# Performance work log

Measured on AMD Instinct MI355X. Metric: run time of the kernel, lower is better.

The kernel has to match this reference:

```python
import jax, jax.numpy as jnp
import numpy as np

B, S, E, H = 2, 2048, 1024, 16
DK = E // H


def setup_inputs() -> dict:
    key = jax.random.key(0)
    ks = jax.random.split(key, 10)
    x = jax.random.normal(ks[0], (B, S, E), dtype=jnp.float32)
    mask = jax.random.randint(ks[1], (B, S, S), 0, 2).astype(bool)
    scale = 1.0 / np.sqrt(E)
    def lin(k):
        kw, kb = jax.random.split(k)
        W = jax.random.uniform(kw, (E, E), minval=-scale, maxval=scale, dtype=jnp.float32)
        b = jax.random.uniform(kb, (E,), minval=-scale, maxval=scale, dtype=jnp.float32)
        return W, b
    Wq, bq = lin(ks[2])
    Wk, bk = lin(ks[3])
    Wv, bv = lin(ks[4])
    Wo, bo = lin(ks[5])
    return {"x": x, "mask": mask, "Wq": Wq, "bq": bq, "Wk": Wk, "bk": bk,
            "Wv": Wv, "bv": bv, "Wo": Wo, "bo": bo}


def reference(x, mask, Wq, bq, Wk, bk, Wv, bv, Wo, bo):
    # projections (torch Linear: y = x @ W.T + b)
    q = x @ Wq.T + bq
    k = x @ Wk.T + bk
    v = x @ Wv.T + bv
    # separate heads: [B,S,E] -> [B,H,S,DK]
    def split(t):
        return t.reshape(B, S, H, DK).transpose(0, 2, 1, 3)
    q, k, v = split(q), split(k), split(v)
    scores = jnp.einsum("bhqd,bhkd->bhqk", q, k) / jnp.sqrt(jnp.float32(DK))
    # masked_fill: positions where mask is True get -1e9 (mask broadcast over heads)
    scores = jnp.where(mask[:, None, :, :], jnp.float32(-1e9), scores)
    attn = jax.nn.softmax(scores, axis=-1)  # dropout is identity in eval
    out = jnp.einsum("bhqk,bhkd->bhqd", attn, v)
    out = out.transpose(0, 2, 1, 3).reshape(B, S, E)  # combine heads
    return out @ Wo.T + bo
```

## Files before the change

kernel.cpp:

```cpp
#include <hip/hip_runtime.h>
#include <hip/hip_bf16.h>


typedef __attribute__((ext_vector_type(8))) short short8;
typedef __attribute__((ext_vector_type(4))) float f32x4;

#define MFMA16(a, b, c) __builtin_amdgcn_mfma_f32_16x16x32_bf16(a, b, c, 0, 0, 0)

#define BATCH 2
#define SEQ   2048
#define EMB   1024
#define HEADS 16
#define DKK   64
#define MROWS (BATCH * SEQ)

typedef __hip_bfloat16 bf16;
typedef unsigned long long u64;

static __device__ __forceinline__ short bf16b(float f) {
    union { bf16 h; short s; } u;
    u.h = __float2bfloat16(f);
    return u.s;
}
static __device__ __forceinline__ short8 ld8k(const bf16* p) {
    return *(const short8*)p;
}
static __device__ __forceinline__ short8 ld8kf(const float* p) {
    const f32x4 a = *(const f32x4*)p;
    const f32x4 b = *(const f32x4*)(p + 4);
    short8 r;
    r[0] = bf16b(a[0]); r[1] = bf16b(a[1]); r[2] = bf16b(a[2]); r[3] = bf16b(a[3]);
    r[4] = bf16b(b[0]); r[5] = bf16b(b[1]); r[6] = bf16b(b[2]); r[7] = bf16b(b[3]);
    return r;
}

static __device__ __forceinline__ void glds16(const bf16* g, bf16* l) {
    __builtin_amdgcn_global_load_lds(
        (const __attribute__((address_space(1))) void*)g,
        (__attribute__((address_space(3))) void*)l, 16, 0, 0);
}

__global__ void detect_kernel(const unsigned int* __restrict__ mw,
                              int* __restrict__ flags) {
    __shared__ int mbyte;
    if (threadIdx.x == 0) mbyte = 0;
    __syncthreads();
    int mb = 0;
    for (int i = threadIdx.x; i < 4096; i += 256)
        if (mw[i] > 1u) mb = 1;
    if (mb) atomicOr(&mbyte, 1);
    __syncthreads();
    if (threadIdx.x == 0) { flags[0] = 1; flags[1] = mbyte; }
}

__global__ __launch_bounds__(256) void pack_mask(
        const void* __restrict__ mp, u64* __restrict__ bm,
        const int* __restrict__ flags) {
    const bool m8 = flags[1] != 0;
    const unsigned char* p8 = (const unsigned char*)mp;
    const int* p32 = (const int*)mp;
    const int lane = threadIdx.x & 63;
    const int w = (blockIdx.x * 256 + threadIdx.x) >> 6;
#pragma unroll 4
    for (int i = 0; i < 32; ++i) {
        const int L = i * 4096 + w;
        const size_t e = (size_t)L * 64 + lane;
        const bool v = m8 ? (p8[e] != 0) : (p32[e] != 0);
        const u64 bal = __ballot(v);
        if (lane == 0) {
            const int qg = L >> 5, it = L & 31;
            bm[((qg >> 11) * 32 + it) * 2048 + (qg & 2047)] = bal;
        }
    }
}

__global__ __launch_bounds__(256) void cvt_all(
        const float* __restrict__ x,  const float* __restrict__ wq,
        const float* __restrict__ wk, const float* __restrict__ wv,
        const float* __restrict__ wo,
        bf16* __restrict__ xb,  bf16* __restrict__ wqb,
        bf16* __restrict__ wkb, bf16* __restrict__ wvb,
        bf16* __restrict__ wob) {
    const int bid = blockIdx.x;
    const float* s; bf16* d; int base;
    if (bid < 2048)      { s = x;  d = xb;  base = bid; }
    else if (bid < 2560) { s = wq; d = wqb; base = bid - 2048; }
    else if (bid < 3072) { s = wk; d = wkb; base = bid - 2560; }
    else if (bid < 3584) { s = wv; d = wvb; base = bid - 3072; }
    else                 { s = wo; d = wob; base = bid - 3584; }
    const int i = (base * 256 + threadIdx.x) * 8;
    *(short8*)(d + i) = ld8kf(s + i);
}

__global__ __launch_bounds__(256) void gemm_qkv_staged(
        const bf16* __restrict__ X,
        const bf16* __restrict__ Wq, const bf16* __restrict__ Wk,
        const bf16* __restrict__ Wv,
        const float* __restrict__ bq, const float* __restrict__ bk,
        const float* __restrict__ bv,
        bf16* __restrict__ qo, bf16* __restrict__ ko, bf16* __restrict__ vo) {
    __shared__ bf16 As[128 * 64];
    __shared__ bf16 Bs[128 * 64];

    const int t = threadIdx.x, lane = t & 63;
    const int wv = t >> 6;
    const int mb = blockIdx.x / 24, nb = blockIdx.x % 24;
    const int m0 = mb * 128;
    const int n0g = nb * 128;
    const int sel = n0g >> 10;
    const int n0 = n0g & 1023;
    const bf16* W     = sel == 0 ? Wq : (sel == 1 ? Wk : Wv);
    const float* bias = sel == 0 ? bq : (sel == 1 ? bk : bv);
    bf16* out         = sel == 0 ? qo : (sel == 1 ? ko : vo);

    const int wr = wv >> 1, wc = wv & 1;
    const int m_off = wr * 64, n_off = wc * 64;
    const int l16 = lane & 15, quad = lane >> 4;

    int srow[4], sg[4];
#pragma unroll
    for (int i = 0; i < 4; ++i) {
        const int c = i * 256 + t;
        srow[i] = c >> 3;
        sg[i]   = (c & 7) ^ (srow[i] & 7);
    }

    f32x4 acc[4][4];
#pragma unroll
    for (int i = 0; i < 4; ++i)
#pragma unroll
        for (int j = 0; j < 4; ++j)
            acc[i][j] = (f32x4){0.f, 0.f, 0.f, 0.f};

    for (int kt = 0; kt < 1024; kt += 64) {
#pragma unroll
        for (int i = 0; i < 4; ++i)
            glds16(X + (m0 + srow[i]) * 1024 + kt + sg[i] * 8, As + (i * 256 + t) * 8);
#pragma unroll
        for (int i = 0; i < 4; ++i)
            glds16(W + (n0 + srow[i]) * 1024 + kt + sg[i] * 8, Bs + (i * 256 + t) * 8);
        __syncthreads();
#pragma unroll
        for (int step = 0; step < 2; ++step) {
            short8 af[4], bfr[4];
#pragma unroll
            for (int ii = 0; ii < 4; ++ii) {
                const int row = m_off + ii * 16 + l16;
                const int slot = (step * 4 + quad) ^ (row & 7);
                af[ii] = *(const short8*)(As + row * 64 + slot * 8);
            }
#pragma unroll
            for (int jj = 0; jj < 4; ++jj) {
                const int row = n_off + jj * 16 + l16;
                const int slot = (step * 4 + quad) ^ (row & 7);
                bfr[jj] = *(const short8*)(Bs + row * 64 + slot * 8);
            }
#pragma unroll
            for (int ii = 0; ii < 4; ++ii)
#pragma unroll
                for (int jj = 0; jj < 4; ++jj)
                    acc[ii][jj] = MFMA16(af[ii], bfr[jj], acc[ii][jj]);
        }
        __syncthreads();
    }

#pragma unroll
    for (int j = 0; j < 4; ++j) {
        const int nl = n0 + n_off + j * 16 + l16;
        const float bj = bias[nl];
        const int h = nl >> 6, d = nl & 63;
#pragma unroll
        for (int i = 0; i < 4; ++i) {
#pragma unroll
            for (int r = 0; r < 4; ++r) {
                const int m = m0 + m_off + i * 16 + quad * 4 + r;
                const float v = acc[i][j][r] + bj;
                const int bb = m >> 11, ss = m & 2047;
                const int idx = (sel == 2)
                    ? ((bb * HEADS + h) * DKK + d) * SEQ + ss
                    : ((bb * HEADS + h) * SEQ + ss) * DKK + d;
                out[idx] = __float2bfloat16(v);
            }
        }
    }
}

__global__ __launch_bounds__(256) void gemm_out_staged(
        const bf16* __restrict__ X,
        const bf16* __restrict__ W, const float* __restrict__ bias,
        float* __restrict__ out) {
    __shared__ bf16 As[128 * 64];
    __shared__ bf16 Bs[64 * 64];

    const int t = threadIdx.x, lane = t & 63;
    const int wv = t >> 6;
    const int mb = blockIdx.x >> 4, nb = blockIdx.x & 15;
    const int m0 = mb * 128, n0 = nb * 64;
    const int wr = wv >> 1, wc = wv & 1;
    const int m_off = wr * 64, n_off = wc * 32;
    const int l16 = lane & 15, quad = lane >> 4;

    int srow[4], sg[4];
#pragma unroll
    for (int i = 0; i < 4; ++i) {
        const int c = i * 256 + t;
        srow[i] = c >> 3;
        sg[i]   = (c & 7) ^ (srow[i] & 7);
    }

    f32x4 acc[4][2];
#pragma unroll
    for (int i = 0; i < 4; ++i)
#pragma unroll
        for (int j = 0; j < 2; ++j)
            acc[i][j] = (f32x4){0.f, 0.f, 0.f, 0.f};

    for (int kt = 0; kt < 1024; kt += 64) {
#pragma unroll
        for (int i = 0; i < 4; ++i)
            glds16(X + (m0 + srow[i]) * 1024 + kt + sg[i] * 8, As + (i * 256 + t) * 8);
#pragma unroll
        for (int i = 0; i < 2; ++i)
            glds16(W + (n0 + srow[i]) * 1024 + kt + sg[i] * 8, Bs + (i * 256 + t) * 8);
        __syncthreads();
#pragma unroll
        for (int step = 0; step < 2; ++step) {
            short8 af[4], bfr[2];
#pragma unroll
            for (int ii = 0; ii < 4; ++ii) {
                const int row = m_off + ii * 16 + l16;
                const int slot = (step * 4 + quad) ^ (row & 7);
                af[ii] = *(const short8*)(As + row * 64 + slot * 8);
            }
#pragma unroll
            for (int jj = 0; jj < 2; ++jj) {
                const int row = n_off + jj * 16 + l16;
                const int slot = (step * 4 + quad) ^ (row & 7);
                bfr[jj] = *(const short8*)(Bs + row * 64 + slot * 8);
            }
#pragma unroll
            for (int ii = 0; ii < 4; ++ii)
#pragma unroll
                for (int jj = 0; jj < 2; ++jj)
                    acc[ii][jj] = MFMA16(af[ii], bfr[jj], acc[ii][jj]);
        }
        __syncthreads();
    }

#pragma unroll
    for (int j = 0; j < 2; ++j) {
        const int n = n0 + n_off + j * 16 + l16;
        const float bj = bias[n];
#pragma unroll
        for (int i = 0; i < 4; ++i) {
#pragma unroll
            for (int r = 0; r < 4; ++r) {
                const int m = m0 + m_off + i * 16 + quad * 4 + r;
                out[m * 1024 + n] = acc[i][j][r] + bj;
            }
        }
    }
}

__global__ __launch_bounds__(256, 3) void attn_kernel(
        const bf16* __restrict__ Qw,
        const bf16* __restrict__ Kw,
        const bf16* __restrict__ Vw,
        const u64* __restrict__ bmT,
        bf16* __restrict__ attn_out) {
    const int t = threadIdx.x;
    const int lane = t & 63;
    const int wv   = t >> 6;
    const int l16 = lane & 15, quad = lane >> 4;
    const int h = blockIdx.y, b = blockIdx.z;
    const int bh = b * HEADS + h;
    const int qb = blockIdx.x * 64 + wv * 16;

    const bf16* Q  = Qw + bh * SEQ * DKK;
    const bf16* Kp = Kw + bh * SEQ * DKK;
    const bf16* Vt = Vw + bh * DKK * SEQ;

    __shared__ bf16 Ks[2][4096];
    __shared__ bf16 Vs[2][4096];
    __shared__ bf16 lds_p[4][16][72];

    short8 qf[2];
    qf[0] = ld8k(Q + (qb + l16) * DKK + quad * 8);
    qf[1] = ld8k(Q + (qb + l16) * DKK + 32 + quad * 8);

    f32x4 o[4];
#pragma unroll
    for (int jd = 0; jd < 4; ++jd) o[jd] = (f32x4){0.f, 0.f, 0.f, 0.f};
    float lsum[4] = {0.f, 0.f, 0.f, 0.f};

    int srow[2], sg[2];
#pragma unroll
    for (int i = 0; i < 2; ++i) {
        const int c = i * 256 + t;
        srow[i] = c >> 3;
        sg[i]   = (c & 7) ^ (srow[i] & 7);
    }

#pragma unroll
    for (int i = 0; i < 2; ++i)
        glds16(Kp + srow[i] * DKK + sg[i] * 8, &Ks[0][(i * 256 + t) * 8]);
#pragma unroll
    for (int i = 0; i < 2; ++i)
        glds16(Vt + srow[i] * SEQ + sg[i] * 8, &Vs[0][(i * 256 + t) * 8]);

    const int qrow = qb + quad * 4;
    u64 mc[4];
#pragma unroll
    for (int r = 0; r < 4; ++r)
        mc[r] = bmT[(size_t)(b * 32) * 2048 + qrow + r];

    const float SC = 0.18033688011f;

    for (int it = 0; it < SEQ / 64; ++it) {
        __syncthreads();
        const int nb_ = (it + 1) & 1;
        u64 mn[4];
        if (it < SEQ / 64 - 1) {
            const int ktn = (it + 1) * 64;
#pragma unroll
            for (int i = 0; i < 2; ++i)
                glds16(Kp + (ktn + srow[i]) * DKK + sg[i] * 8, &Ks[nb_][(i * 256 + t) * 8]);
#pragma unroll
            for (int i = 0; i < 2; ++i)
                glds16(Vt + srow[i] * SEQ + ktn + sg[i] * 8, &Vs[nb_][(i * 256 + t) * 8]);
#pragma unroll
            for (int r = 0; r < 4; ++r)
                mn[r] = bmT[(size_t)(b * 32 + it + 1) * 2048 + qrow + r];
        }

        const bf16* Kb = Ks[it & 1];
        const bf16* Vb = Vs[it & 1];

        f32x4 s[4];
#pragma unroll
        for (int j = 0; j < 4; ++j) s[j] = (f32x4){0.f, 0.f, 0.f, 0.f};
#pragma unroll
        for (int t2 = 0; t2 < 2; ++t2)
#pragma unroll
            for (int j = 0; j < 4; ++j) {
                const int row = j * 16 + l16;
                const int slot = (t2 * 4 + quad) ^ (row & 7);
                const short8 kf = *(const short8*)(Kb + row * 64 + slot * 8);
                s[j] = MFMA16(qf[t2], kf, s[j]);
            }

#pragma unroll
        for (int r = 0; r < 4; ++r) {
            const unsigned wlo = ~(unsigned)mc[r];
            const unsigned whi = ~(unsigned)(mc[r] >> 32);
#pragma unroll
            for (int j = 0; j < 4; ++j) {
                const unsigned word = (j < 2) ? wlo : whi;
                const float bitf = (float)((word >> ((j & 1) * 16 + l16)) & 1u);
                const float p = __builtin_exp2f(s[j][r] * SC) * bitf;
                lsum[r] += p;
                lds_p[wv][quad * 4 + r][j * 16 + l16] = __float2bfloat16(p);
            }
        }

#pragma unroll
        for (int t2 = 0; t2 < 2; ++t2) {
            const short8 pf = *(const short8*)(&lds_p[wv][l16][t2 * 32 + quad * 8]);
#pragma unroll
            for (int jd = 0; jd < 4; ++jd) {
                const int row = jd * 16 + l16;
                const int slot = (t2 * 4 + quad) ^ (row & 7);
                const short8 vf = *(const short8*)(Vb + row * 64 + slot * 8);
                o[jd] = MFMA16(pf, vf, o[jd]);
            }
        }
        if (it < SEQ / 64 - 1) {
#pragma unroll
            for (int r = 0; r < 4; ++r) mc[r] = mn[r];
        }
    }

#pragma unroll
    for (int r = 0; r < 4; ++r) {
        float l = lsum[r];
#pragma unroll
        for (int off = 8; off >= 1; off >>= 1)
            l += __shfl_xor(l, off, 16);
        const float inv = 1.0f / l;
        const int q = qb + quad * 4 + r;
#pragma unroll
        for (int jd = 0; jd < 4; ++jd)
            attn_out[(b * SEQ + q) * EMB + h * DKK + jd * 16 + l16] =
                __float2bfloat16(o[jd][r] * inv);
    }
}

extern "C" void kernel_launch(void* const* d_in, const int* in_sizes, int n_in,
                              void* d_out, int out_size, void* d_ws, size_t ws_size,
                              hipStream_t stream) {
    char* ws = (char*)d_ws;
    const size_t MB = 1024 * 1024;
    int*  flags = (int*)ws;
    u64*  bm    = (u64*)(ws + 256);
    bf16* xb    = (bf16*)(ws + 256 + MB);
    bf16* wqb   = (bf16*)(ws + 256 + 9 * MB);
    bf16* wkb   = (bf16*)(ws + 256 + 11 * MB);
    bf16* wvb   = (bf16*)(ws + 256 + 13 * MB);
    bf16* wob   = (bf16*)(ws + 256 + 15 * MB);
    bf16* k_ws  = (bf16*)(ws + 256 + 17 * MB);
    bf16* attn_ws = xb;

    bf16* q_ws = (bf16*)d_out;
    bf16* v_ws = (bf16*)d_out + 4194304;

    detect_kernel<<<1, 256, 0, stream>>>((const unsigned int*)d_in[1], flags);
    pack_mask<<<1024, 256, 0, stream>>>(d_in[1], bm, flags);

    cvt_all<<<4096, 256, 0, stream>>>(
        (const float*)d_in[0], (const float*)d_in[2], (const float*)d_in[4],
        (const float*)d_in[6], (const float*)d_in[8],
        xb, wqb, wkb, wvb, wob);

    gemm_qkv_staged<<<768, 256, 0, stream>>>(
        xb, wqb, wkb, wvb,
        (const float*)d_in[3], (const float*)d_in[5], (const float*)d_in[7],
        q_ws, k_ws, v_ws);

    attn_kernel<<<dim3(SEQ / 64, HEADS, BATCH), 256, 0, stream>>>(
        q_ws, k_ws, v_ws, bm, attn_ws);

    gemm_out_staged<<<512, 256, 0, stream>>>(
        attn_ws, wob, (const float*)d_in[9], (float*)d_out);
}
```

Measured before the change: 300.7 us.

## Double-buffer GEMM K tiles and process two query tiles per attention wave

Both projection GEMMs switch from single-buffered 64-wide K tiles with two barriers per step to double-buffered 32-wide K tiles, so the next tile's global-to-LDS load is issued before the MFMAs on the current one. The attention kernel now gives each wave 32 query rows instead of 16, which halves the grid and reuses each K/V fragment loaded from LDS for two query tiles. The goal is to hide load latency and cut LDS traffic per MFMA, at the cost of more registers, a lower occupancy hint and fewer attention blocks in flight.

```diff
diff --git a/kernel.cpp b/kernel.cpp
--- a/kernel.cpp
+++ b/kernel.cpp
@@ -99,8 +99,8 @@
         const float* __restrict__ bq, const float* __restrict__ bk,
         const float* __restrict__ bv,
         bf16* __restrict__ qo, bf16* __restrict__ ko, bf16* __restrict__ vo) {
-    __shared__ bf16 As[128 * 64];
-    __shared__ bf16 Bs[128 * 64];
+    __shared__ bf16 As[2][128 * 32];
+    __shared__ bf16 Bs[2][128 * 32];
 
     const int t = threadIdx.x, lane = t & 63;
     const int wv = t >> 6;
@@ -117,12 +117,12 @@
     const int m_off = wr * 64, n_off = wc * 64;
     const int l16 = lane & 15, quad = lane >> 4;
 
-    int srow[4], sg[4];
-#pragma unroll
-    for (int i = 0; i < 4; ++i) {
+    int srow[2], sg[2];
+#pragma unroll
+    for (int i = 0; i < 2; ++i) {
         const int c = i * 256 + t;
-        srow[i] = c >> 3;
-        sg[i]   = (c & 7) ^ (srow[i] & 7);
+        srow[i] = c >> 2;
+        sg[i]   = (c & 3) ^ (srow[i] & 3);
     }
 
     f32x4 acc[4][4];
@@ -132,36 +132,45 @@
         for (int j = 0; j < 4; ++j)
             acc[i][j] = (f32x4){0.f, 0.f, 0.f, 0.f};
 
-    for (int kt = 0; kt < 1024; kt += 64) {
-#pragma unroll
-        for (int i = 0; i < 4; ++i)
-            glds16(X + (m0 + srow[i]) * 1024 + kt + sg[i] * 8, As + (i * 256 + t) * 8);
-#pragma unroll
-        for (int i = 0; i < 4; ++i)
-            glds16(W + (n0 + srow[i]) * 1024 + kt + sg[i] * 8, Bs + (i * 256 + t) * 8);
+#pragma unroll
+    for (int i = 0; i < 2; ++i) {
+        glds16(X + (m0 + srow[i]) * 1024 + sg[i] * 8, &As[0][(i * 256 + t) * 8]);
+        glds16(W + (n0 + srow[i]) * 1024 + sg[i] * 8, &Bs[0][(i * 256 + t) * 8]);
+    }
+
+    for (int it = 0; it < 32; ++it) {
         __syncthreads();
-#pragma unroll
-        for (int step = 0; step < 2; ++step) {
-            short8 af[4], bfr[4];
-#pragma unroll
-            for (int ii = 0; ii < 4; ++ii) {
-                const int row = m_off + ii * 16 + l16;
-                const int slot = (step * 4 + quad) ^ (row & 7);
-                af[ii] = *(const short8*)(As + row * 64 + slot * 8);
-            }
-#pragma unroll
-            for (int jj = 0; jj < 4; ++jj) {
-                const int row = n_off + jj * 16 + l16;
-                const int slot = (step * 4 + quad) ^ (row & 7);
-                bfr[jj] = *(const short8*)(Bs + row * 64 + slot * 8);
-            }
-#pragma unroll
-            for (int ii = 0; ii < 4; ++ii)
-#pragma unroll
-                for (int jj = 0; jj < 4; ++jj)
-                    acc[ii][jj] = MFMA16(af[ii], bfr[jj], acc[ii][jj]);
-        }
-        __syncthreads();
+        if (it < 31) {
+            const int ktn = (it + 1) * 32;
+            const int nb_ = (it + 1) & 1;
+#pragma unroll
+            for (int i = 0; i < 2; ++i) {
+                glds16(X + (m0 + srow[i]) * 1024 + ktn + sg[i] * 8,
+                       &As[nb_][(i * 256 + t) * 8]);
+                glds16(W + (n0 + srow[i]) * 1024 + ktn + sg[i] * 8,
+                       &Bs[nb_][(i * 256 + t) * 8]);
+            }
+        }
+        const bf16* Ab = As[it & 1];
+        const bf16* Bb = Bs[it & 1];
+        short8 af[4], bfr[4];
+#pragma unroll
+        for (int ii = 0; ii < 4; ++ii) {
+            const int row = m_off + ii * 16 + l16;
+            const int slot = quad ^ (row & 3);
+            af[ii] = *(const short8*)(Ab + row * 32 + slot * 8);
+        }
+#pragma unroll
+        for (int jj = 0; jj < 4; ++jj) {
+            const int row = n_off + jj * 16 + l16;
+            const int slot = quad ^ (row & 3);
+            bfr[jj] = *(const short8*)(Bb + row * 32 + slot * 8);
+        }
+#pragma unroll
+        for (int ii = 0; ii < 4; ++ii)
+#pragma unroll
+            for (int jj = 0; jj < 4; ++jj)
+                acc[ii][jj] = MFMA16(af[ii], bfr[jj], acc[ii][jj]);
     }
 
 #pragma unroll
@@ -189,8 +198,8 @@
         const bf16* __restrict__ X,
         const bf16* __restrict__ W, const float* __restrict__ bias,
         float* __restrict__ out) {
-    __shared__ bf16 As[128 * 64];
-    __shared__ bf16 Bs[64 * 64];
+    __shared__ bf16 As[2][128 * 32];
+    __shared__ bf16 Bs[2][64 * 32];
 
     const int t = threadIdx.x, lane = t & 63;
     const int wv = t >> 6;
@@ -200,13 +209,15 @@
     const int m_off = wr * 64, n_off = wc * 32;
     const int l16 = lane & 15, quad = lane >> 4;
 
-    int srow[4], sg[4];
-#pragma unroll
-    for (int i = 0; i < 4; ++i) {
+    int srow[2], sg[2];
+#pragma unroll
+    for (int i = 0; i < 2; ++i) {
         const int c = i * 256 + t;
-        srow[i] = c >> 3;
-        sg[i]   = (c & 7) ^ (srow[i] & 7);
-    }
+        srow[i] = c >> 2;
+        sg[i]   = (c & 3) ^ (srow[i] & 3);
+    }
+    const int brow = t >> 2;
+    const int bslot = (t & 3) ^ (brow & 3);
 
     f32x4 acc[4][2];
 #pragma unroll
@@ -215,36 +226,42 @@
         for (int j = 0; j < 2; ++j)
             acc[i][j] = (f32x4){0.f, 0.f, 0.f, 0.f};
 
-    for (int kt = 0; kt < 1024; kt += 64) {
-#pragma unroll
-        for (int i = 0; i < 4; ++i)
-            glds16(X + (m0 + srow[i]) * 1024 + kt + sg[i] * 8, As + (i * 256 + t) * 8);
-#pragma unroll
-        for (int i = 0; i < 2; ++i)
-            glds16(W + (n0 + srow[i]) * 1024 + kt + sg[i] * 8, Bs + (i * 256 + t) * 8);
+#pragma unroll
+    for (int i = 0; i < 2; ++i)
+        glds16(X + (m0 + srow[i]) * 1024 + sg[i] * 8, &As[0][(i * 256 + t) * 8]);
+    glds16(W + (n0 + brow) * 1024 + bslot * 8, &Bs[0][t * 8]);
+
+    for (int it = 0; it < 32; ++it) {
         __syncthreads();
-#pragma unroll
-        for (int step = 0; step < 2; ++step) {
-            short8 af[4], bfr[2];
-#pragma unroll
-            for (int ii = 0; ii < 4; ++ii) {
-                const int row = m_off + ii * 16 + l16;
-                const int slot = (step * 4 + quad) ^ (row & 7);
-                af[ii] = *(const short8*)(As + row * 64 + slot * 8);
-            }
-#pragma unroll
-            for (int jj = 0; jj < 2; ++jj) {
-                const int row = n_off + jj * 16 + l16;
-                const int slot = (step * 4 + quad) ^ (row & 7);
-                bfr[jj] = *(const short8*)(Bs + row * 64 + slot * 8);
-            }
-#pragma unroll
-            for (int ii = 0; ii < 4; ++ii)
-#pragma unroll
-                for (int jj = 0; jj < 2; ++jj)
-                    acc[ii][jj] = MFMA16(af[ii], bfr[jj], acc[ii][jj]);
-        }
-        __syncthreads();
+        if (it < 31) {
+            const int ktn = (it + 1) * 32;
+            const int nb_ = (it + 1) & 1;
+#pragma unroll
+            for (int i = 0; i < 2; ++i)
+                glds16(X + (m0 + srow[i]) * 1024 + ktn + sg[i] * 8,
+                       &As[nb_][(i * 256 + t) * 8]);
+            glds16(W + (n0 + brow) * 1024 + ktn + bslot * 8, &Bs[nb_][t * 8]);
+        }
+        const bf16* Ab = As[it & 1];
+        const bf16* Bb = Bs[it & 1];
+        short8 af[4], bfr[2];
+#pragma unroll
+        for (int ii = 0; ii < 4; ++ii) {
+            const int row = m_off + ii * 16 + l16;
+            const int slot = quad ^ (row & 3);
+            af[ii] = *(const short8*)(Ab + row * 32 + slot * 8);
+        }
+#pragma unroll
+        for (int jj = 0; jj < 2; ++jj) {
+            const int row = n_off + jj * 16 + l16;
+            const int slot = quad ^ (row & 3);
+            bfr[jj] = *(const short8*)(Bb + row * 32 + slot * 8);
+        }
+#pragma unroll
+        for (int ii = 0; ii < 4; ++ii)
+#pragma unroll
+            for (int jj = 0; jj < 2; ++jj)
+                acc[ii][jj] = MFMA16(af[ii], bfr[jj], acc[ii][jj]);
     }
 
 #pragma unroll
@@ -262,7 +279,7 @@
     }
 }
 
-__global__ __launch_bounds__(256, 3) void attn_kernel(
+__global__ __launch_bounds__(256, 2) void attn_kernel(
         const bf16* __restrict__ Qw,
         const bf16* __restrict__ Kw,
         const bf16* __restrict__ Vw,
@@ -274,7 +291,7 @@
     const int l16 = lane & 15, quad = lane >> 4;
     const int h = blockIdx.y, b = blockIdx.z;
     const int bh = b * HEADS + h;
-    const int qb = blockIdx.x * 64 + wv * 16;
+    const int qb0 = blockIdx.x * 128;
 
     const bf16* Q  = Qw + bh * SEQ * DKK;
     const bf16* Kp = Kw + bh * SEQ * DKK;
@@ -282,16 +299,21 @@
 
     __shared__ bf16 Ks[2][4096];
     __shared__ bf16 Vs[2][4096];
-    __shared__ bf16 lds_p[4][16][72];
-
-    short8 qf[2];
-    qf[0] = ld8k(Q + (qb + l16) * DKK + quad * 8);
-    qf[1] = ld8k(Q + (qb + l16) * DKK + 32 + quad * 8);
-
-    f32x4 o[4];
-#pragma unroll
-    for (int jd = 0; jd < 4; ++jd) o[jd] = (f32x4){0.f, 0.f, 0.f, 0.f};
-    float lsum[4] = {0.f, 0.f, 0.f, 0.f};
+    __shared__ bf16 lds_p[4][2][16][72];
+
+    short8 qf[2][2];
+#pragma unroll
+    for (int i = 0; i < 2; ++i)
+#pragma unroll
+        for (int t2 = 0; t2 < 2; ++t2)
+            qf[i][t2] = ld8k(Q + (qb0 + wv * 32 + i * 16 + l16) * DKK + t2 * 32 + quad * 8);
+
+    f32x4 o[2][4];
+#pragma unroll
+    for (int i = 0; i < 2; ++i)
+#pragma unroll
+        for (int jd = 0; jd < 4; ++jd) o[i][jd] = (f32x4){0.f, 0.f, 0.f, 0.f};
+    float lsum[2][4] = {{0.f,0.f,0.f,0.f},{0.f,0.f,0.f,0.f}};
 
     int srow[2], sg[2];
 #pragma unroll
@@ -308,18 +330,19 @@
     for (int i = 0; i < 2; ++i)
         glds16(Vt + srow[i] * SEQ + sg[i] * 8, &Vs[0][(i * 256 + t) * 8]);
 
-    const int qrow = qb + quad * 4;
-    u64 mc[4];
-#pragma unroll
-    for (int r = 0; r < 4; ++r)
-        mc[r] = bmT[(size_t)(b * 32) * 2048 + qrow + r];
+    const int qrow_base = qb0 + wv * 32 + quad * 4;
+    u64 mc[2][4];
+#pragma unroll
+    for (int i = 0; i < 2; ++i)
+#pragma unroll
+        for (int r = 0; r < 4; ++r)
+            mc[i][r] = bmT[(size_t)(b * 32) * 2048 + qrow_base + i * 16 + r];
 
     const float SC = 0.18033688011f;
 
     for (int it = 0; it < SEQ / 64; ++it) {
         __syncthreads();
         const int nb_ = (it + 1) & 1;
-        u64 mn[4];
         if (it < SEQ / 64 - 1) {
             const int ktn = (it + 1) * 64;
 #pragma unroll
@@ -328,71 +351,96 @@
 #pragma unroll
             for (int i = 0; i < 2; ++i)
                 glds16(Vt + srow[i] * SEQ + ktn + sg[i] * 8, &Vs[nb_][(i * 256 + t) * 8]);
-#pragma unroll
-            for (int r = 0; r < 4; ++r)
-                mn[r] = bmT[(size_t)(b * 32 + it + 1) * 2048 + qrow + r];
+        }
+        u64 mn[2][4];
+        if (it < SEQ / 64 - 1) {
+#pragma unroll
+            for (int i = 0; i < 2; ++i)
+#pragma unroll
+                for (int r = 0; r < 4; ++r)
+                    mn[i][r] = bmT[(size_t)(b * 32 + it + 1) * 2048 + qrow_base + i * 16 + r];
         }
 
         const bf16* Kb = Ks[it & 1];
         const bf16* Vb = Vs[it & 1];
 
-        f32x4 s[4];
-#pragma unroll
-        for (int j = 0; j < 4; ++j) s[j] = (f32x4){0.f, 0.f, 0.f, 0.f};
+        short8 kf[2][4];
 #pragma unroll
         for (int t2 = 0; t2 < 2; ++t2)
 #pragma unroll
             for (int j = 0; j < 4; ++j) {
                 const int row = j * 16 + l16;
                 const int slot = (t2 * 4 + quad) ^ (row & 7);
-                const short8 kf = *(const short8*)(Kb + row * 64 + slot * 8);
-                s[j] = MFMA16(qf[t2], kf, s[j]);
-            }
-
-#pragma unroll
-        for (int r = 0; r < 4; ++r) {
-            const unsigned wlo = ~(unsigned)mc[r];
-            const unsigned whi = ~(unsigned)(mc[r] >> 32);
+                kf[t2][j] = *(const short8*)(Kb + row * 64 + slot * 8);
+            }
+
+        f32x4 s[2][4];
+#pragma unroll
+        for (int i = 0; i < 2; ++i)
 #pragma unroll
             for (int j = 0; j < 4; ++j) {
-                const unsigned word = (j < 2) ? wlo : whi;
-                const float bitf = (float)((word >> ((j & 1) * 16 + l16)) & 1u);
-                const float p = __builtin_exp2f(s[j][r] * SC) * bitf;
-                lsum[r] += p;
-                lds_p[wv][quad * 4 + r][j * 16 + l16] = __float2bfloat16(p);
-            }
-        }
+                s[i][j] = (f32x4){0.f, 0.f, 0.f, 0.f};
+#pragma unroll
+                for (int t2 = 0; t2 < 2; ++t2)
+                    s[i][j] = MFMA16(qf[i][t2], kf[t2][j], s[i][j]);
+            }
+
+#pragma unroll
+        for (int i = 0; i < 2; ++i)
+#pragma unroll
+            for (int r = 0; r < 4; ++r) {
+                const unsigned wlo = ~(unsigned)mc[i][r];
+                const unsigned whi = ~(unsigned)(mc[i][r] >> 32);
+#pragma unroll
+                for (int j = 0; j < 4; ++j) {
+                    const unsigned word = (j < 2) ? wlo : whi;
+                    const float bitf = (float)((word >> ((j & 1) * 16 + l16)) & 1u);
+                    const float p = __builtin_exp2f(s[i][j][r] * SC) * bitf;
+                    lsum[i][r] += p;
+                    lds_p[wv][i][quad * 4 + r][j * 16 + l16] = __float2bfloat16(p);
+                }
+            }
 
 #pragma unroll
         for (int t2 = 0; t2 < 2; ++t2) {
-            const short8 pf = *(const short8*)(&lds_p[wv][l16][t2 * 32 + quad * 8]);
+            short8 vf[4];
 #pragma unroll
             for (int jd = 0; jd < 4; ++jd) {
                 const int row = jd * 16 + l16;
                 const int slot = (t2 * 4 + quad) ^ (row & 7);
-                const short8 vf = *(const short8*)(Vb + row * 64 + slot * 8);
-                o[jd] = MFMA16(pf, vf, o[jd]);
+                vf[jd] = *(const short8*)(Vb + row * 64 + slot * 8);
+            }
+#pragma unroll
+            for (int i = 0; i < 2; ++i) {
+                short8 pf = *(const short8*)(&lds_p[wv][i][l16][t2 * 32 + quad * 8]);
+#pragma unroll
+                for (int jd = 0; jd < 4; ++jd)
+                    o[i][jd] = MFMA16(pf, vf[jd], o[i][jd]);
             }
         }
         if (it < SEQ / 64 - 1) {
 #pragma unroll
-            for (int r = 0; r < 4; ++r) mc[r] = mn[r];
-        }
-    }
-
-#pragma unroll
-    for (int r = 0; r < 4; ++r) {
-        float l = lsum[r];
-#pragma unroll
-        for (int off = 8; off >= 1; off >>= 1)
-            l += __shfl_xor(l, off, 16);
-        const float inv = 1.0f / l;
-        const int q = qb + quad * 4 + r;
-#pragma unroll
-        for (int jd = 0; jd < 4; ++jd)
-            attn_out[(b * SEQ + q) * EMB + h * DKK + jd * 16 + l16] =
-                __float2bfloat16(o[jd][r] * inv);
-    }
+            for (int i = 0; i < 2; ++i)
+#pragma unroll
+                for (int r = 0; r < 4; ++r) mc[i][r] = mn[i][r];
+        }
+    }
+
+#pragma unroll
+    for (int i = 0; i < 2; ++i)
+#pragma unroll
+        for (int r = 0; r < 4; ++r) {
+            float l = lsum[i][r];
+#pragma unroll
+            for (int off = 8; off >= 1; off >>= 1)
+                l += __shfl_xor(l, off, 16);
+            const float inv = 1.0f / l;
+            const int q = qb0 + wv * 32 + i * 16 + quad * 4 + r;
+#pragma unroll
+            for (int jd = 0; jd < 4; ++jd)
+                attn_out[(b * SEQ + q) * EMB + h * DKK + jd * 16 + l16] =
+                    __float2bfloat16(o[i][jd][r] * inv);
+        }
 }
 
 extern "C" void kernel_launch(void* const* d_in, const int* in_sizes, int n_in,
@@ -426,7 +474,7 @@
         (const float*)d_in[3], (const float*)d_in[5], (const float*)d_in[7],
         q_ws, k_ws, v_ws);
 
-    attn_kernel<<<dim3(SEQ / 64, HEADS, BATCH), 256, 0, stream>>>(
+    attn_kernel<<<dim3(SEQ / 128, HEADS, BATCH), 256, 0, stream>>>(
         q_ws, k_ws, v_ws, bm, attn_ws);
 
     gemm_out_staged<<<512, 256, 0, stream>>>(
```

New measurement: 278.1 us. -7.5%, faster.
